# Performance work log

Measured on AMD Instinct MI355X. Metric: run time of the kernel, lower is better.

The kernel has to match this reference:

```python
import jax, jax.numpy as jnp
import numpy as np

D_MODEL = 1024
N_HEADS = 16
D_HEAD = D_MODEL // N_HEADS
HIDDEN = 4096
B, T = 2, 2048
EPS = 1e-5


def setup_inputs() -> dict:
    key = jax.random.key(0)
    ks = jax.random.split(key, 16)
    s = 0.02
    return {
        "x": jax.random.normal(ks[0], (B, T, D_MODEL), dtype=jnp.float32),
        # LayerNorm 1
        "gamma1": jnp.ones((D_MODEL,), jnp.float32),
        "beta1": jnp.zeros((D_MODEL,), jnp.float32),
        # attention projections, stored (in, out) so y = x @ W + b
        "Wq": jax.random.normal(ks[1], (D_MODEL, D_MODEL), jnp.float32) * s,
        "bq": jnp.zeros((D_MODEL,), jnp.float32),
        "Wk": jax.random.normal(ks[2], (D_MODEL, D_MODEL), jnp.float32) * s,
        "bk": jnp.zeros((D_MODEL,), jnp.float32),
        "Wv": jax.random.normal(ks[3], (D_MODEL, D_MODEL), jnp.float32) * s,
        "bv": jnp.zeros((D_MODEL,), jnp.float32),
        "Wo": jax.random.normal(ks[4], (D_MODEL, D_MODEL), jnp.float32) * s,
        "bo": jnp.zeros((D_MODEL,), jnp.float32),
        # LayerNorm 2
        "gamma2": jnp.ones((D_MODEL,), jnp.float32),
        "beta2": jnp.zeros((D_MODEL,), jnp.float32),
        # MLP
        "W1": jax.random.normal(ks[5], (D_MODEL, HIDDEN), jnp.float32) * s,
        "b1": jnp.zeros((HIDDEN,), jnp.float32),
        "W2": jax.random.normal(ks[6], (HIDDEN, D_MODEL), jnp.float32) * s,
        "b2": jnp.zeros((D_MODEL,), jnp.float32),
    }


def _layernorm(x, gamma, beta):
    mean = jnp.mean(x, axis=-1, keepdims=True)
    var = jnp.mean(jnp.square(x - mean), axis=-1, keepdims=True)  # unbiased=False
    return gamma * (x - mean) * jax.lax.rsqrt(var + EPS) + beta


def _attention(x, Wq, bq, Wk, bk, Wv, bv, Wo, bo):
    b, t, _ = x.shape
    q = (x @ Wq + bq).reshape(b, t, N_HEADS, D_HEAD)
    k = (x @ Wk + bk).reshape(b, t, N_HEADS, D_HEAD)
    v = (x @ Wv + bv).reshape(b, t, N_HEADS, D_HEAD)
    scores = jnp.einsum("bqhd,bkhd->bhqk", q, k) / np.sqrt(D_HEAD).astype(np.float32)
    causal = jnp.tril(jnp.ones((t, t), dtype=bool))  # keep j <= i
    scores = jnp.where(causal, scores, -jnp.inf)
    attn = jax.nn.softmax(scores, axis=-1)
    out = jnp.einsum("bhqk,bkhd->bqhd", attn, v).reshape(b, t, D_MODEL)
    return out @ Wo + bo


def reference(x, gamma1, beta1, Wq, bq, Wk, bk, Wv, bv, Wo, bo,
              gamma2, beta2, W1, b1, W2, b2):
    # x = x + Attn(LN1(x))
    x = x + _attention(_layernorm(x, gamma1, beta1), Wq, bq, Wk, bk, Wv, bv, Wo, bo)
    # x = x + MLP(LN2(x)); torch F.gelu default = exact erf gelu
    h = _layernorm(x, gamma2, beta2)
    h = jax.nn.gelu(h @ W1 + b1, approximate=False) @ W2 + b2
    return x + h
```

## Files before the change

### kernel.cpp

```cpp
#include <hip/hip_runtime.h>
#include <stdint.h>

typedef unsigned short u16;
typedef short bf16x8 __attribute__((ext_vector_type(8)));
typedef float f32x4 __attribute__((ext_vector_type(4)));
typedef float f32x16 __attribute__((ext_vector_type(16)));

#define MB (1024L*1024L)

__device__ inline u16 f2bf(float f) {
  union { float f; unsigned u; } v; v.f = f;
  unsigned r = (v.u + 0x7FFFu + ((v.u >> 16) & 1u)) >> 16;
  return (u16)r;
}

__device__ inline unsigned cvtpk(float lo, float hi) {
  unsigned r;
  asm("v_cvt_pk_bf16_f32 %0, %1, %2" : "=v"(r) : "v"(lo), "v"(hi));
  return r;
}

#define GLOAD16(gptr, lptr) \
  __builtin_amdgcn_global_load_lds((__attribute__((address_space(1))) void*)(gptr), \
                                   (__attribute__((address_space(3))) void*)(lptr), 16, 0, 0)

__global__ __launch_bounds__(256) void twconv(const float* __restrict__ W,
                                              u16* __restrict__ WT, int K, int N) {
  __shared__ float tile[32][33];
  const int nbn = N >> 5;
  const int bk = blockIdx.x / nbn;
  const int bn = blockIdx.x % nbn;
  const int tid = threadIdx.x;
  const int r = tid >> 3;
  const int c4 = (tid & 7) << 2;
  const float4 v = *(const float4*)(W + (size_t)(bk * 32 + r) * N + bn * 32 + c4);
  tile[r][c4 + 0] = v.x; tile[r][c4 + 1] = v.y;
  tile[r][c4 + 2] = v.z; tile[r][c4 + 3] = v.w;
  __syncthreads();
  ushort4 o;
  o.x = f2bf(tile[c4 + 0][r]); o.y = f2bf(tile[c4 + 1][r]);
  o.z = f2bf(tile[c4 + 2][r]); o.w = f2bf(tile[c4 + 3][r]);
  *(ushort4*)(WT + (size_t)(bn * 32 + r) * K + bk * 32 + c4) = o;
}

__global__ __launch_bounds__(256) void concat3(const float* __restrict__ a,
                                               const float* __restrict__ b,
                                               const float* __restrict__ c,
                                               float* __restrict__ out, int n) {
  int i = blockIdx.x * 256 + threadIdx.x;
  if (i < n) { out[i] = a[i]; out[n + i] = b[i]; out[2 * n + i] = c[i]; }
}

__global__ __launch_bounds__(256) void ln_kernel(const float* __restrict__ x,
                                                 const float* __restrict__ gamma,
                                                 const float* __restrict__ beta,
                                                 u16* __restrict__ out) {
  const int row = blockIdx.x;
  const int tid = threadIdx.x;
  const float4 v = *(const float4*)(x + (size_t)row * 1024 + tid * 4);
  float s = v.x + v.y + v.z + v.w;
  float s2 = v.x * v.x + v.y * v.y + v.z * v.z + v.w * v.w;
#pragma unroll
  for (int m = 1; m < 64; m <<= 1) {
    s += __shfl_xor(s, m, 64);
    s2 += __shfl_xor(s2, m, 64);
  }
  __shared__ float red[8];
  const int w = tid >> 6;
  if ((tid & 63) == 0) { red[w] = s; red[4 + w] = s2; }
  __syncthreads();
  s = red[0] + red[1] + red[2] + red[3];
  s2 = red[4] + red[5] + red[6] + red[7];
  const float mean = s * (1.0f / 1024.0f);
  const float var = s2 * (1.0f / 1024.0f) - mean * mean;
  const float rstd = rsqrtf(var + 1e-5f);
  const float4 g = *(const float4*)(gamma + tid * 4);
  const float4 b = *(const float4*)(beta + tid * 4);
  ushort4 o;
  o.x = f2bf(g.x * (v.x - mean) * rstd + b.x);
  o.y = f2bf(g.y * (v.y - mean) * rstd + b.y);
  o.z = f2bf(g.z * (v.z - mean) * rstd + b.z);
  o.w = f2bf(g.w * (v.w - mean) * rstd + b.w);
  *(ushort4*)(out + (size_t)row * 1024 + tid * 4) = o;
}

template <int EPI, int BN>
__global__ __launch_bounds__(256, (BN == 64) ? 3 : 2)
void gemm_bt(const u16* __restrict__ A, const u16* __restrict__ BT,
             const float* __restrict__ bias, const float* __restrict__ res,
             void* __restrict__ outp, int M, int N, int K) {
  constexpr int MF = (BN == 128) ? 4 : 2;
  constexpr int ACH = 4;
  constexpr int BCH = BN / 32;
  constexpr int LOADS = ACH + BCH;
  __shared__ __align__(16) u16 As[2][128 * 64];
  __shared__ __align__(16) u16 Bs[2][BN * 64];
  const int nBN = N / BN;
  const int bm = blockIdx.x / nBN;
  const int bn = blockIdx.x % nBN;
  const int tid = threadIdx.x;
  const int lane = tid & 63;
  const int wid = tid >> 6;
  const int wm = (BN == 128) ? (wid >> 1) : wid;
  const int wn = (BN == 128) ? (wid & 1) : 0;
  const int e4 = lane >> 4;

  int abase[MF], ax[MF];
#pragma unroll
  for (int m = 0; m < MF; ++m) {
    int rowa = wm * (MF * 16) + m * 16 + (lane & 15);
    abase[m] = rowa * 64; ax[m] = rowa & 7;
  }
  int bbase[4], bx[4];
#pragma unroll
  for (int n = 0; n < 4; ++n) {
    int rowb = wn * 64 + n * 16 + (lane & 15);
    bbase[n] = rowb * 64; bx[n] = rowb & 7;
  }

  size_t ga[ACH]; int loa[ACH];
#pragma unroll
  for (int c = 0; c < ACH; ++c) {
    int idx = tid + (c << 8);
    int row = idx >> 3;
    int ch = (idx & 7) ^ (row & 7);
    ga[c] = (size_t)(bm * 128 + row) * K + (ch << 3);
    loa[c] = idx << 4;
  }
  size_t gb[BCH]; int lob[BCH];
#pragma unroll
  for (int c = 0; c < BCH; ++c) {
    int idx = tid + (c << 8);
    int row = idx >> 3;
    int ch = (idx & 7) ^ (row & 7);
    gb[c] = (size_t)(bn * BN + row) * K + (ch << 3);
    lob[c] = idx << 4;
  }

#define STAGE_G(t, bb) do { \
  _Pragma("unroll") for (int c = 0; c < ACH; ++c) \
    GLOAD16(A + ga[c] + (size_t)(t) * 64, (char*)As[bb] + loa[c]); \
  _Pragma("unroll") for (int c = 0; c < BCH; ++c) \
    GLOAD16(BT + gb[c] + (size_t)(t) * 64, (char*)Bs[bb] + lob[c]); \
} while (0)

  f32x4 acc[MF][4] = {};
  const int nt = K >> 6;

  STAGE_G(0, 0);
  STAGE_G(1, 1);

  for (int t = 0; t < nt; ++t) {
    if (t + 1 < nt) {
      asm volatile("s_waitcnt vmcnt(%0)" :: "i"(LOADS) : "memory");
    } else {
      asm volatile("s_waitcnt vmcnt(0)" ::: "memory");
    }
    __builtin_amdgcn_s_barrier();
    const u16* Ap = As[t & 1];
    const u16* Bp = Bs[t & 1];
    bf16x8 af[2][MF], bfr[2][4];
#pragma unroll
    for (int kk = 0; kk < 2; ++kk) {
#pragma unroll
      for (int m = 0; m < MF; ++m)
        af[kk][m] = *(const bf16x8*)(Ap + abase[m] + (((((kk << 2) | e4)) ^ ax[m]) << 3));
#pragma unroll
      for (int n = 0; n < 4; ++n)
        bfr[kk][n] = *(const bf16x8*)(Bp + bbase[n] + (((((kk << 2) | e4)) ^ bx[n]) << 3));
    }
    asm volatile("s_waitcnt lgkmcnt(0)" ::: "memory");
    __builtin_amdgcn_s_barrier();
    if (t + 2 < nt) STAGE_G(t + 2, t & 1);
    __builtin_amdgcn_s_setprio(1);
#pragma unroll
    for (int kk = 0; kk < 2; ++kk)
#pragma unroll
      for (int m = 0; m < MF; ++m)
#pragma unroll
        for (int n = 0; n < 4; ++n)
          acc[m][n] = __builtin_amdgcn_mfma_f32_16x16x32_bf16(af[kk][m], bfr[kk][n], acc[m][n], 0, 0, 0);
    __builtin_amdgcn_s_setprio(0);
  }
#undef STAGE_G

  const int rbase = bm * 128 + wm * (MF * 16);
  const int cbase = bn * BN + wn * 64;
#pragma unroll
  for (int m = 0; m < MF; ++m) {
#pragma unroll
    for (int n = 0; n < 4; ++n) {
      const int col = cbase + n * 16 + (lane & 15);
      const int row0 = rbase + m * 16 + ((lane >> 4) << 2);
      const float bv = bias[col];
#pragma unroll
      for (int r = 0; r < 4; ++r) {
        const int row = row0 + r;
        float v = acc[m][n][r] + bv;
        if (EPI == 1) {
          ((float*)outp)[(size_t)row * N + col] = v + res[(size_t)row * N + col];
        } else if (EPI == 2) {
          float tt = v * (1.0f + 0.044715f * v * v);
          float sg = 1.0f / (1.0f + __expf(-1.5957691216057308f * tt));
          ((u16*)outp)[(size_t)row * N + col] = f2bf(v * sg);
        } else {
          ((u16*)outp)[(size_t)row * N + col] = f2bf(v);
        }
      }
    }
  }
}

__global__ __launch_bounds__(512, 2) void attn_kernel(const u16* __restrict__ QKV,
                                                      u16* __restrict__ O) {
  __shared__ __align__(16) u16 KV[4][4096];
  const int T = 2048, LD = 3072;
  const int p = blockIdx.x & 7;
  const int bh = blockIdx.x >> 3;
  const int b = bh >> 4, hd = bh & 15;
  const int tid = threadIdx.x;
  const int lane = tid & 63;
  const int w = tid >> 6;
  const int h = lane >> 5;
  const int cA = p, cB = 15 - p;
  const int myc = (w < 4) ? cA : cB;
  const int qwb = myc * 128 + (w & 3) * 32;
  const int qg = qwb + (lane & 31);
  const int diag = qwb >> 6;
  const int myNt = diag + 1;
  const int nt = 2 * cB + 2;

  const u16* Qb = QKV + (size_t)b * T * LD + hd * 64;
  const u16* Kb = Qb + 1024;
  const u16* Vb = Qb + 2048;

  bf16x8 qf[4];
#pragma unroll
  for (int s = 0; s < 4; ++s)
    qf[s] = *(const bf16x8*)(Qb + (size_t)qg * LD + s * 16 + h * 8);

  f32x16 oacc[2] = {};
  float m = -INFINITY, l = 0.0f;

  const int srow = tid >> 3;
  const int scol = tid & 7;
  const int kgc = ((scol ^ (srow & 7)) << 3);

  GLOAD16(Kb + (size_t)srow * LD + kgc, (char*)KV[0] + tid * 16);
  {
    bf16x8 vv0 = *(const bf16x8*)(Vb + (size_t)srow * LD + scol * 8);
#pragma unroll
    for (int e = 0; e < 8; ++e) {
      int d = scol * 8 + e;
      KV[2][(d << 6) | (srow & 7) | ((((srow >> 3) ^ e ^ scol) & 7) << 3)] = (u16)vv0[e];
    }
  }
  __syncthreads();

  int cur = 0;
  for (int j = 0; j < nt; ++j) {
    const bool pre = (j + 1 < nt);
    bf16x8 vv;
    if (pre) {
      GLOAD16(Kb + (size_t)((j + 1) * 64 + srow) * LD + kgc, (char*)KV[cur ^ 1] + tid * 16);
      vv = *(const bf16x8*)(Vb + (size_t)((j + 1) * 64 + srow) * LD + scol * 8);
    }

    if (j < myNt) {
      f32x16 sacc[2] = {};
      const u16* Kp = KV[cur];
#pragma unroll
      for (int t = 0; t < 2; ++t) {
#pragma unroll
        for (int s = 0; s < 4; ++s) {
          int row = t * 32 + (lane & 31);
          bf16x8 kf = *(const bf16x8*)(Kp + (row << 6) + ((((2 * s + h) ^ (row & 7)) & 7) << 3));
          sacc[t] = __builtin_amdgcn_mfma_f32_32x32x16_bf16(kf, qf[s], sacc[t], 0, 0, 0);
        }
      }

      if (j == diag) {
#pragma unroll
        for (int t = 0; t < 2; ++t)
#pragma unroll
          for (int r = 0; r < 16; ++r) {
            int key = (j << 6) + 32 * t + (r & 3) + 8 * (r >> 2) + 4 * h;
            if (key > qg) sacc[t][r] = -INFINITY;
          }
      }

      float pmax = -INFINITY;
#pragma unroll
      for (int t = 0; t < 2; ++t)
#pragma unroll
        for (int r = 0; r < 16; ++r) pmax = fmaxf(pmax, sacc[t][r]);
      pmax = fmaxf(pmax, __shfl_xor(pmax, 32, 64));

      if (!__all(pmax - m <= 16.0f)) {
        float mn = fmaxf(m, pmax);
        float alpha = __expf(0.125f * (m - mn));
        m = mn;
        l *= alpha;
#pragma unroll
        for (int d2 = 0; d2 < 2; ++d2)
#pragma unroll
          for (int r = 0; r < 16; ++r) oacc[d2][r] *= alpha;
      }

      float lsum = 0.0f;
#pragma unroll
      for (int t = 0; t < 2; ++t)
#pragma unroll
        for (int r = 0; r < 16; ++r) {
          float pe = __expf(0.125f * (sacc[t][r] - m));
          sacc[t][r] = pe;
          lsum += pe;
        }
      lsum += __shfl_xor(lsum, 32, 64);
      l += lsum;

      union PF { unsigned wd[4]; bf16x8 v; } pf[4];
#pragma unroll
      for (int t = 0; t < 2; ++t) {
#pragma unroll
        for (int kb = 0; kb < 2; ++kb) {
          int base = 8 * kb;
          unsigned A0 = cvtpk(sacc[t][base + 0], sacc[t][base + 1]);
          unsigned A2 = cvtpk(sacc[t][base + 2], sacc[t][base + 3]);
          unsigned A4 = cvtpk(sacc[t][base + 4], sacc[t][base + 5]);
          unsigned A6 = cvtpk(sacc[t][base + 6], sacc[t][base + 7]);
          unsigned S0 = (unsigned)__shfl_xor((int)(h ? A0 : A4), 32, 64);
          unsigned S2 = (unsigned)__shfl_xor((int)(h ? A2 : A6), 32, 64);
          PF& u = pf[2 * t + kb];
          u.wd[0] = h ? S0 : A0;
          u.wd[1] = h ? S2 : A2;
          u.wd[2] = h ? A4 : S0;
          u.wd[3] = h ? A6 : S2;
        }
      }

      const u16* Vp = KV[2 + cur];
#pragma unroll
      for (int d2 = 0; d2 < 2; ++d2) {
        int d = d2 * 32 + (lane & 31);
#pragma unroll
        for (int ks = 0; ks < 4; ++ks) {
          bf16x8 vf = *(const bf16x8*)(Vp + (d << 6) + ((((2 * ks + h) ^ (d & 7) ^ ((d >> 3) & 7)) & 7) << 3));
          oacc[d2] = __builtin_amdgcn_mfma_f32_32x32x16_bf16(vf, pf[ks].v, oacc[d2], 0, 0, 0);
        }
      }
    }

    if (pre) {
#pragma unroll
      for (int e = 0; e < 8; ++e) {
        int d = scol * 8 + e;
        KV[2 + (cur ^ 1)][(d << 6) | (srow & 7) | ((((srow >> 3) ^ e ^ scol) & 7) << 3)] = (u16)vv[e];
      }
    }
    __syncthreads();
    cur ^= 1;
  }

  const float rinv = 1.0f / l;
  u16* Ob = (u16*)KV;
  const int qloc = w * 32 + (lane & 31);
#pragma unroll
  for (int d2 = 0; d2 < 2; ++d2)
#pragma unroll
    for (int r = 0; r < 16; ++r) {
      int d = d2 * 32 + (r & 3) + 8 * (r >> 2) + 4 * h;
      Ob[(qloc << 6) | (d ^ ((qloc & 7) << 3))] = f2bf(oacc[d2][r] * rinv);
    }
  __syncthreads();
#pragma unroll
  for (int it = 0; it < 4; ++it) {
    int r = (tid >> 3) + it * 64;
    int c = tid & 7;
    bf16x8 val = *(const bf16x8*)(Ob + (r << 6) + (((c ^ (r & 7)) & 7) << 3));
    int qg2 = (r < 128) ? (cA * 128 + r) : (cB * 128 + (r - 128));
    *(bf16x8*)(O + (size_t)(b * T + qg2) * 1024 + hd * 64 + c * 8) = val;
  }
}

extern "C" void kernel_launch(void* const* d_in, const int* in_sizes, int n_in,
                              void* d_out, int out_size, void* d_ws, size_t ws_size,
                              hipStream_t stream) {
  const float* x      = (const float*)d_in[0];
  const float* gamma1 = (const float*)d_in[1];
  const float* beta1  = (const float*)d_in[2];
  const float* Wq     = (const float*)d_in[3];
  const float* bq     = (const float*)d_in[4];
  const float* Wk     = (const float*)d_in[5];
  const float* bk     = (const float*)d_in[6];
  const float* Wv     = (const float*)d_in[7];
  const float* bv     = (const float*)d_in[8];
  const float* Wo     = (const float*)d_in[9];
  const float* bo     = (const float*)d_in[10];
  const float* gamma2 = (const float*)d_in[11];
  const float* beta2  = (const float*)d_in[12];
  const float* W1     = (const float*)d_in[13];
  const float* b1     = (const float*)d_in[14];
  const float* W2     = (const float*)d_in[15];
  const float* b2     = (const float*)d_in[16];

  char* ws = (char*)d_ws;
  u16* WqkvT = (u16*)(ws + 0 * MB);
  u16* WoT   = (u16*)(ws + 6 * MB);
  u16* W1T   = (u16*)(ws + 8 * MB);
  u16* W2T   = (u16*)(ws + 16 * MB);
  u16* qkv   = (u16*)(ws + 24 * MB);
  u16* hb    = (u16*)(ws + 24 * MB);
  u16* xn    = (u16*)(ws + 56 * MB);
  float* bqkv = (float*)d_out;
  float* x1 = (float*)d_out;

  const int M = 4096;

  twconv<<<dim3(1024), dim3(256), 0, stream>>>(Wq, WqkvT, 1024, 1024);
  twconv<<<dim3(1024), dim3(256), 0, stream>>>(Wk, WqkvT + 1024 * 1024, 1024, 1024);
  twconv<<<dim3(1024), dim3(256), 0, stream>>>(Wv, WqkvT + 2048 * 1024, 1024, 1024);
  twconv<<<dim3(1024), dim3(256), 0, stream>>>(Wo, WoT, 1024, 1024);
  twconv<<<dim3(4096), dim3(256), 0, stream>>>(W1, W1T, 1024, 4096);
  twconv<<<dim3(4096), dim3(256), 0, stream>>>(W2, W2T, 4096, 1024);
  concat3<<<dim3(4), dim3(256), 0, stream>>>(bq, bk, bv, bqkv, 1024);

  ln_kernel<<<dim3(M), dim3(256), 0, stream>>>(x, gamma1, beta1, xn);

  gemm_bt<0, 128><<<dim3(768), dim3(256), 0, stream>>>(xn, WqkvT, bqkv, nullptr, qkv, M, 3072, 1024);

  attn_kernel<<<dim3(256), dim3(512), 0, stream>>>(qkv, xn);

  gemm_bt<1, 64><<<dim3(512), dim3(256), 0, stream>>>(xn, WoT, bo, x, x1, M, 1024, 1024);

  ln_kernel<<<dim3(M), dim3(256), 0, stream>>>(x1, gamma2, beta2, xn);

  gemm_bt<2, 128><<<dim3(1024), dim3(256), 0, stream>>>(xn, W1T, b1, nullptr, hb, M, 4096, 1024);
  gemm_bt<1, 64><<<dim3(512), dim3(256), 0, stream>>>(hb, W2T, b2, x1, d_out, M, 1024, 4096);
}
```

Before: 239.5 us.

## Split attention into smaller 256-thread blocks, fold scale into Q, remap blocks per XCD

The attention kernel now uses 256-thread blocks covering two 64-row query chunks, with 512 blocks instead of 256. Each thread loads two K/V rows per tile. Q is pre-scaled by log2(e)/sqrt(d) so softmax can use exp2 with no per-element multiply, and the rescale threshold is adjusted to match. Block indices in the GEMM and attention kernels are remapped so consecutive row tiles and heads land on the same XCD for better L2 locality. The risks are the extra Q rounding step and whether the GEMM remap still fits every grid size.

After: 254.3 us. +6.2%, slower.

```diff
diff --git a/kernel.cpp b/kernel.cpp
--- a/kernel.cpp
+++ b/kernel.cpp
@@ -12,6 +12,10 @@
   union { float f; unsigned u; } v; v.f = f;
   unsigned r = (v.u + 0x7FFFu + ((v.u >> 16) & 1u)) >> 16;
   return (u16)r;
+}
+
+__device__ inline float bf2f(u16 u) {
+  union { unsigned u; float f; } v; v.u = ((unsigned)u) << 16; return v.f;
 }
 
 __device__ inline unsigned cvtpk(float lo, float hi) {
@@ -96,8 +100,11 @@
   __shared__ __align__(16) u16 As[2][128 * 64];
   __shared__ __align__(16) u16 Bs[2][BN * 64];
   const int nBN = N / BN;
-  const int bm = blockIdx.x / nBN;
-  const int bn = blockIdx.x % nBN;
+  const int hw = blockIdx.x;
+  const int xcd = hw & 7;
+  const int rr = hw >> 3;
+  const int bm = xcd * 4 + rr / nBN;
+  const int bn = rr % nBN;
   const int tid = threadIdx.x;
   const int lane = tid & 63;
   const int wid = tid >> 6;
@@ -211,48 +218,64 @@
   }
 }
 
-__global__ __launch_bounds__(512, 2) void attn_kernel(const u16* __restrict__ QKV,
+__global__ __launch_bounds__(256, 3) void attn_kernel(const u16* __restrict__ QKV,
                                                       u16* __restrict__ O) {
   __shared__ __align__(16) u16 KV[4][4096];
   const int T = 2048, LD = 3072;
-  const int p = blockIdx.x & 7;
-  const int bh = blockIdx.x >> 3;
+  const int hw = blockIdx.x;
+  const int xcd = hw & 7;
+  const int rr = hw >> 3;
+  const int bh = xcd + 8 * (rr >> 4);
+  const int p = rr & 15;
   const int b = bh >> 4, hd = bh & 15;
   const int tid = threadIdx.x;
   const int lane = tid & 63;
   const int w = tid >> 6;
   const int h = lane >> 5;
-  const int cA = p, cB = 15 - p;
-  const int myc = (w < 4) ? cA : cB;
-  const int qwb = myc * 128 + (w & 3) * 32;
+  const int cA = p, cB = 31 - p;
+  const int myc = (w < 2) ? cA : cB;
+  const int qwb = myc * 64 + (w & 1) * 32;
   const int qg = qwb + (lane & 31);
-  const int diag = qwb >> 6;
-  const int myNt = diag + 1;
-  const int nt = 2 * cB + 2;
+  const int myNt = myc + 1;
+  const int nt = cB + 1;
 
   const u16* Qb = QKV + (size_t)b * T * LD + hd * 64;
   const u16* Kb = Qb + 1024;
   const u16* Vb = Qb + 2048;
 
+  const float QSC = 0.18033688011112042f;
   bf16x8 qf[4];
 #pragma unroll
-  for (int s = 0; s < 4; ++s)
-    qf[s] = *(const bf16x8*)(Qb + (size_t)qg * LD + s * 16 + h * 8);
+  for (int s = 0; s < 4; ++s) {
+    bf16x8 raw = *(const bf16x8*)(Qb + (size_t)qg * LD + s * 16 + h * 8);
+    union { unsigned wd[4]; bf16x8 v; } u;
+#pragma unroll
+    for (int e = 0; e < 4; ++e)
+      u.wd[e] = cvtpk(bf2f((u16)raw[2 * e]) * QSC, bf2f((u16)raw[2 * e + 1]) * QSC);
+    qf[s] = u.v;
+  }
 
   f32x16 oacc[2] = {};
   float m = -INFINITY, l = 0.0f;
 
-  const int srow = tid >> 3;
-  const int scol = tid & 7;
-  const int kgc = ((scol ^ (srow & 7)) << 3);
-
-  GLOAD16(Kb + (size_t)srow * LD + kgc, (char*)KV[0] + tid * 16);
-  {
-    bf16x8 vv0 = *(const bf16x8*)(Vb + (size_t)srow * LD + scol * 8);
+  int krow[2], kgc[2], vrow[2], vcol[2];
+#pragma unroll
+  for (int c2 = 0; c2 < 2; ++c2) {
+    int idx = tid + (c2 << 8);
+    krow[c2] = idx >> 3;
+    kgc[c2] = ((idx & 7) ^ (krow[c2] & 7)) << 3;
+    vrow[c2] = idx >> 3;
+    vcol[c2] = idx & 7;
+  }
+
+#pragma unroll
+  for (int c2 = 0; c2 < 2; ++c2) {
+    GLOAD16(Kb + (size_t)krow[c2] * LD + kgc[c2], (char*)KV[0] + (tid + (c2 << 8)) * 16);
+    bf16x8 vv0 = *(const bf16x8*)(Vb + (size_t)vrow[c2] * LD + vcol[c2] * 8);
 #pragma unroll
     for (int e = 0; e < 8; ++e) {
-      int d = scol * 8 + e;
-      KV[2][(d << 6) | (srow & 7) | ((((srow >> 3) ^ e ^ scol) & 7) << 3)] = (u16)vv0[e];
+      int d = vcol[c2] * 8 + e;
+      KV[2][(d << 6) | (vrow[c2] & 7) | ((((vrow[c2] >> 3) ^ e ^ vcol[c2]) & 7) << 3)] = (u16)vv0[e];
     }
   }
   __syncthreads();
@@ -260,10 +283,14 @@
   int cur = 0;
   for (int j = 0; j < nt; ++j) {
     const bool pre = (j + 1 < nt);
-    bf16x8 vv;
+    bf16x8 vv[2];
     if (pre) {
-      GLOAD16(Kb + (size_t)((j + 1) * 64 + srow) * LD + kgc, (char*)KV[cur ^ 1] + tid * 16);
-      vv = *(const bf16x8*)(Vb + (size_t)((j + 1) * 64 + srow) * LD + scol * 8);
+#pragma unroll
+      for (int c2 = 0; c2 < 2; ++c2) {
+        GLOAD16(Kb + (size_t)((j + 1) * 64 + krow[c2]) * LD + kgc[c2],
+                (char*)KV[cur ^ 1] + (tid + (c2 << 8)) * 16);
+        vv[c2] = *(const bf16x8*)(Vb + (size_t)((j + 1) * 64 + vrow[c2]) * LD + vcol[c2] * 8);
+      }
     }
 
     if (j < myNt) {
@@ -279,7 +306,7 @@
         }
       }
 
-      if (j == diag) {
+      if (j == myc) {
 #pragma unroll
         for (int t = 0; t < 2; ++t)
 #pragma unroll
@@ -296,9 +323,9 @@
         for (int r = 0; r < 16; ++r) pmax = fmaxf(pmax, sacc[t][r]);
       pmax = fmaxf(pmax, __shfl_xor(pmax, 32, 64));
 
-      if (!__all(pmax - m <= 16.0f)) {
+      if (!__all(pmax - m <= 2.8853900817779268f)) {
         float mn = fmaxf(m, pmax);
-        float alpha = __expf(0.125f * (m - mn));
+        float alpha = exp2f(m - mn);
         m = mn;
         l *= alpha;
 #pragma unroll
@@ -312,7 +339,7 @@
       for (int t = 0; t < 2; ++t)
 #pragma unroll
         for (int r = 0; r < 16; ++r) {
-          float pe = __expf(0.125f * (sacc[t][r] - m));
+          float pe = exp2f(sacc[t][r] - m);
           sacc[t][r] = pe;
           lsum += pe;
         }
@@ -353,10 +380,12 @@
 
     if (pre) {
 #pragma unroll
-      for (int e = 0; e < 8; ++e) {
-        int d = scol * 8 + e;
-        KV[2 + (cur ^ 1)][(d << 6) | (srow & 7) | ((((srow >> 3) ^ e ^ scol) & 7) << 3)] = (u16)vv[e];
-      }
+      for (int c2 = 0; c2 < 2; ++c2)
+#pragma unroll
+        for (int e = 0; e < 8; ++e) {
+          int d = vcol[c2] * 8 + e;
+          KV[2 + (cur ^ 1)][(d << 6) | (vrow[c2] & 7) | ((((vrow[c2] >> 3) ^ e ^ vcol[c2]) & 7) << 3)] = (u16)vv[c2][e];
+        }
     }
     __syncthreads();
     cur ^= 1;
@@ -375,10 +404,10 @@
   __syncthreads();
 #pragma unroll
   for (int it = 0; it < 4; ++it) {
-    int r = (tid >> 3) + it * 64;
+    int r = (tid >> 3) + it * 32;
     int c = tid & 7;
     bf16x8 val = *(const bf16x8*)(Ob + (r << 6) + (((c ^ (r & 7)) & 7) << 3));
-    int qg2 = (r < 128) ? (cA * 128 + r) : (cB * 128 + (r - 128));
+    int qg2 = (r < 64) ? (cA * 64 + r) : (cB * 64 + (r - 64));
     *(bf16x8*)(O + (size_t)(b * T + qg2) * 1024 + hd * 64 + c * 8) = val;
   }
 }
@@ -429,7 +458,7 @@
 
   gemm_bt<0, 128><<<dim3(768), dim3(256), 0, stream>>>(xn, WqkvT, bqkv, nullptr, qkv, M, 3072, 1024);
 
-  attn_kernel<<<dim3(256), dim3(512), 0, stream>>>(qkv, xn);
+  attn_kernel<<<dim3(512), dim3(256), 0, stream>>>(qkv, xn);
 
   gemm_bt<1, 64><<<dim3(512), dim3(256), 0, stream>>>(xn, WoT, bo, x, x1, M, 1024, 1024);
 
```
